# Kernel tuning notes

Hardware: AMD Instinct MI355X
Metric: run time of the kernel (lower is better)

The kernel has to match this reference:

```python
import jax, jax.numpy as jnp
import numpy as np

EPS = 1e-5
OFFSET_SCALE = 1.0
KPTS = 9   # 3x3 deformable kernel
GROUP = 1  # in_dim // out_dim


def _bn(x, g, b, m, v):
    # eval-mode BatchNorm2d on (B,C,H,W)
    s = g / jnp.sqrt(v + EPS)
    return x * s[None, :, None, None] + (b - m * s)[None, :, None, None]


def _dcnv4_core(value, offset, mask, offset_scale):
    # value: (B,H,W,G,Cg); offset: (B,H,W,G,K,2) as (dx,dy); mask: (B,H,W,G,K)
    B, H, W, G, Cg = value.shape
    K = mask.shape[-1]
    dt = value.dtype
    ky = jnp.repeat(jnp.arange(3) - 1, 3).astype(dt)
    kx = jnp.tile(jnp.arange(3) - 1, 3).astype(dt)
    grid = jnp.stack([kx, ky], -1)                                   # (K,2)
    base = jnp.stack(jnp.meshgrid(jnp.arange(W, dtype=dt),
                                  jnp.arange(H, dtype=dt),
                                  indexing='xy'), -1)                # (H,W,2) = (x,y)
    loc = base[None, :, :, None, None, :] + (grid + offset) * offset_scale  # (B,H,W,G,K,2)
    px, py = loc[..., 0], loc[..., 1]
    x0 = jnp.floor(px); y0 = jnp.floor(py)
    fx = px - x0; fy = py - y0
    vflat = value.transpose(0, 3, 1, 2, 4).reshape(B, G, H * W, Cg)
    out = jnp.zeros((B, G, H * W, Cg), dt)
    corners = ((0.0, 0.0, (1 - fx) * (1 - fy)), (1.0, 0.0, fx * (1 - fy)),
               (0.0, 1.0, (1 - fx) * fy), (1.0, 1.0, fx * fy))
    for dx, dy, wgt in corners:
        xi = x0 + dx; yi = y0 + dy
        valid = ((xi >= 0) & (xi < W) & (yi >= 0) & (yi < H)).astype(dt)
        idx = (jnp.clip(yi, 0, W and H - 1) * W + jnp.clip(xi, 0, W - 1)).astype(jnp.int32)
        idx = idx.transpose(0, 3, 1, 2, 4).reshape(B, G, H * W * K)
        v = jnp.take_along_axis(vflat, idx[..., None], axis=2).reshape(B, G, H * W, K, Cg)
        w = (wgt * valid * mask).transpose(0, 3, 1, 2, 4).reshape(B, G, H * W, K)
        out = out + jnp.einsum('bgsk,bgskc->bgsc', w, v)
    return out.reshape(B, G, H, W, Cg).transpose(0, 2, 3, 1, 4).reshape(B, H, W, G * Cg)


def setup_inputs() -> dict:
    key = jax.random.key(0)
    B, C, H, W = 8, 128, 64, 64
    C_OUT = 128
    OM = ((GROUP * KPTS * 3 + 7) // 8) * 8  # 32, offset_mask padded width
    ks = jax.random.split(key, 16)
    f = jnp.float32
    sc = 1.0 / np.sqrt(C).astype(np.float32)
    return {
        'x': jax.random.normal(ks[0], (B, C, H, W), f),
        'bn1_g': jax.random.uniform(ks[1], (C,), f, 0.5, 1.5),
        'bn1_b': jax.random.normal(ks[2], (C,), f) * 0.1,
        'bn1_m': jax.random.normal(ks[3], (C,), f) * 0.1,
        'bn1_v': jax.random.uniform(ks[4], (C,), f, 0.5, 1.5),
        'w_pw0': jax.random.normal(ks[5], (C, C), f) * sc,
        'w_vp': jax.random.normal(ks[6], (C, C), f) * sc,
        'b_vp': jnp.zeros((C,), f),
        'w_om': jax.random.normal(ks[7], (C, OM), f) * 0.01,
        'b_om': jnp.zeros((OM,), f),
        'w_op': jax.random.normal(ks[8], (C, C), f) * sc,
        'bn2_g': jax.random.uniform(ks[9], (C,), f, 0.5, 1.5),
        'bn2_b': jax.random.normal(ks[10], (C,), f) * 0.1,
        'bn2_m': jax.random.normal(ks[11], (C,), f) * 0.1,
        'bn2_v': jax.random.uniform(ks[12], (C,), f, 0.5, 1.5),
        'w_pw1': jax.random.normal(ks[13], (C_OUT, C), f) * sc,
    }


def reference(x, bn1_g, bn1_b, bn1_m, bn1_v, w_pw0, w_vp, b_vp, w_om, b_om, w_op,
              bn2_g, bn2_b, bn2_m, bn2_v, w_pw1):
    x = _bn(x, bn1_g, bn1_b, bn1_m, bn1_v)
    x = jnp.einsum('bchw,oc->bohw', x, w_pw0)
    B, C, H, W = x.shape
    x = x.reshape(B, H * W, C)  # raw reshape (faithful to torch .reshape, NOT a permute)
    G, K = GROUP, KPTS
    Cg = C // G
    value = (x @ w_vp + b_vp).reshape(B, H, W, G, Cg)
    om = (x @ w_om + b_om)[..., :G * K * 3].reshape(B, H, W, G, K, 3)
    out = _dcnv4_core(value, om[..., :2], om[..., 2], OFFSET_SCALE)
    out = out.reshape(B, H * W, C) @ w_op
    x = out.reshape(B, C, H, W)  # raw reshape back
    x = _bn(x, bn2_g, bn2_b, bn2_m, bn2_v)
    x = jnp.einsum('bchw,oc->bohw', x, w_pw1)
    return x
```

## Files before the change

### kernel.cpp

```cpp
#include <hip/hip_runtime.h>

#define HW 4096
#define PADF 33
#define PADU 136
typedef unsigned short ushort;
typedef __attribute__((ext_vector_type(8))) short short8;
typedef __attribute__((ext_vector_type(4))) float f32x4;

__device__ __forceinline__ ushort bf_rne(float f) {
  unsigned u = __float_as_uint(f);
  unsigned r = (u + 0x7fffu + ((u >> 16) & 1u)) >> 16;
  return (ushort)r;
}
__device__ __forceinline__ void split2(float f, ushort& hi, ushort& lo) {
  ushort h = bf_rne(f);
  float hf = __uint_as_float((unsigned)h << 16);
  hi = h;
  lo = bf_rne(f - hf);
}

__global__ __launch_bounds__(256) void prep(
    const float* __restrict__ g1, const float* __restrict__ be1,
    const float* __restrict__ m1, const float* __restrict__ v1,
    const float* __restrict__ w0,
    const float* __restrict__ g2, const float* __restrict__ be2,
    const float* __restrict__ m2, const float* __restrict__ v2,
    const float* __restrict__ w1,
    const float* __restrict__ wvp, const float* __restrict__ wom,
    const float* __restrict__ wop,
    ushort* __restrict__ W0h, ushort* __restrict__ W0l, float* __restrict__ b0,
    ushort* __restrict__ W1h, ushort* __restrict__ W1l, float* __restrict__ b1,
    ushort* __restrict__ vph, ushort* __restrict__ vpl,
    ushort* __restrict__ oph, ushort* __restrict__ opl,
    ushort* __restrict__ omh, ushort* __restrict__ oml)
{
  const int t = threadIdx.x;
  const int role = blockIdx.x;
  if (role < 16) {
    __shared__ float sc[128], sh[128], part[16][17];
    const int cv = role >> 3;
    const float* g  = cv ? g2 : g1;
    const float* be = cv ? be2 : be1;
    const float* mm = cv ? m2 : m1;
    const float* vv = cv ? v2 : v1;
    if (t < 128) {
      float s = g[t] / sqrtf(vv[t] + 1e-5f);
      sc[t] = s;
      sh[t] = be[t] - mm[t] * s;
    }
    __syncthreads();
    const float* ws = cv ? w1 : w0;
    ushort* dh = cv ? W1h : W0h;
    ushort* dl = cv ? W1l : W0l;
    float* bb  = cv ? b1 : b0;
    const int o = ((role & 7) << 4) + (t >> 4);
    const int kl = t & 15;
    float accb = 0.f;
    #pragma unroll
    for (int j = 0; j < 8; ++j) {
      const int k = (kl << 3) + j;
      const float wv = ws[o * 128 + k];
      ushort hi, lo;
      split2(wv * sc[k], hi, lo);
      dh[o * 128 + k] = hi;
      dl[o * 128 + k] = lo;
      accb = fmaf(wv, sh[k], accb);
    }
    part[t >> 4][kl] = accb;
    __syncthreads();
    if (kl == 0) {
      float s = 0.f;
      #pragma unroll
      for (int j = 0; j < 16; ++j) s += part[t >> 4][j];
      bb[o] = s;
    }
  } else if (role < 32) {
    const int rr = role & 7;
    const float* srcM = (role < 24) ? wvp : wop;
    ushort* dh = (role < 24) ? vph : oph;
    ushort* dl = (role < 24) ? vpl : opl;
    const int n = (rr << 4) + (t >> 4);
    const int kl = t & 15;
    #pragma unroll
    for (int j = 0; j < 8; ++j) {
      const int k = (kl << 3) + j;
      ushort hi, lo;
      split2(srcM[k * 128 + n], hi, lo);
      dh[n * 128 + k] = hi;
      dl[n * 128 + k] = lo;
    }
  } else {
    const int n = ((role - 32) << 4) + (t >> 4);
    const int kl = t & 15;
    #pragma unroll
    for (int j = 0; j < 8; ++j) {
      const int k = (kl << 3) + j;
      ushort hi, lo;
      split2(wom[k * 32 + n], hi, lo);
      omh[n * 128 + k] = hi;
      oml[n * 128 + k] = lo;
    }
  }
}

__global__ __launch_bounds__(256, 2) void fused_x_valom(
    const float* __restrict__ x,
    const ushort* __restrict__ W0h, const ushort* __restrict__ W0l,
    const float* __restrict__ b0,
    const ushort* __restrict__ vph, const ushort* __restrict__ vpl,
    const float* __restrict__ bvp, const float* __restrict__ bom,
    float* __restrict__ value, float* __restrict__ omb)
{
  __shared__ __align__(16) char smem[55296];
  __shared__ float b0_s[64], b2_s[160];
  ushort (*Wh_s)[32] = (ushort(*)[32])(smem);
  ushort (*Wl_s)[32] = (ushort(*)[32])(smem + 4096);
  float*  Xf         = (float*)(smem + 8192);
  ushort (*Yh)[PADU] = (ushort(*)[PADU])(smem);
  ushort (*Yl)[PADU] = (ushort(*)[PADU])(smem + 17408);
  ushort (*Vh_s)[32] = (ushort(*)[32])(smem + 34816);
  ushort (*Vl_s)[32] = (ushort(*)[32])(smem + 45056);

  const int t = threadIdx.x;
  const int cb = blockIdx.x;
  const int b  = blockIdx.y;
  const int oBase = blockIdx.z << 6;
  const int hwBase = cb << 7;
  const size_t xbase = (size_t)b * (size_t)(128 * HW);
  if (t < 64)  b0_s[t] = b0[oBase + t];
  if (t < 160) b2_s[t] = (t < 128) ? bvp[t] : bom[t - 128];
  const int lane = t & 63, w = t >> 6;
  const int col = lane & 15, quad = lane >> 4;
  const f32x4 z = {0.f, 0.f, 0.f, 0.f};

  f32x4 acc1[4][2];
  #pragma unroll
  for (int i = 0; i < 4; ++i) { acc1[i][0] = z; acc1[i][1] = z; }

  for (int kc = 0; kc < 4; ++kc) {
    const int kB = kc << 5;
    {
      const int o = t >> 2, q8 = (t & 3) << 3;
      *(uint4*)&Wh_s[o][q8] = *(const uint4*)&W0h[(oBase + o) * 128 + kB + q8];
      *(uint4*)&Wl_s[o][q8] = *(const uint4*)&W0l[(oBase + o) * 128 + kB + q8];
    }
    #pragma unroll
    for (int p = 0; p < 4; ++p) {
      const int idx = (p << 8) + t;
      const int c = idx >> 5, j4 = (idx & 31) << 2;
      const float4 f = *(const float4*)&x[xbase + (size_t)(kB + c) * HW + hwBase + j4];
      Xf[(j4 + 0) * PADF + c] = f.x;
      Xf[(j4 + 1) * PADF + c] = f.y;
      Xf[(j4 + 2) * PADF + c] = f.z;
      Xf[(j4 + 3) * PADF + c] = f.w;
    }
    __syncthreads();
    union { ushort u[8]; short8 v; } bh[2], bl[2];
    #pragma unroll
    for (int g = 0; g < 2; ++g) {
      const float* xr = &Xf[((w << 5) + (g << 4) + col) * PADF + (quad << 3)];
      #pragma unroll
      for (int j = 0; j < 8; ++j) split2(xr[j], bh[g].u[j], bl[g].u[j]);
    }
    #pragma unroll
    for (int f = 0; f < 4; ++f) {
      const int row = (f << 4) + col;
      const short8 aH = *(const short8*)&Wh_s[row][quad << 3];
      const short8 aL = *(const short8*)&Wl_s[row][quad << 3];
      #pragma unroll
      for (int g = 0; g < 2; ++g) {
        acc1[f][g] = __builtin_amdgcn_mfma_f32_16x16x32_bf16(aH, bh[g].v, acc1[f][g], 0, 0, 0);
        acc1[f][g] = __builtin_amdgcn_mfma_f32_16x16x32_bf16(aH, bl[g].v, acc1[f][g], 0, 0, 0);
        acc1[f][g] = __builtin_amdgcn_mfma_f32_16x16x32_bf16(aL, bh[g].v, acc1[f][g], 0, 0, 0);
      }
    }
    __syncthreads();
  }

  #pragma unroll
  for (int f = 0; f < 4; ++f)
    #pragma unroll
    for (int r = 0; r < 4; ++r) {
      const int m = (f << 4) + (quad << 2) + r;
      #pragma unroll
      for (int g = 0; g < 2; ++g) {
        const int j = (w << 5) + (g << 4) + col;
        ushort hi, lo;
        split2(acc1[f][g][r] + b0_s[m], hi, lo);
        Yh[m][j] = hi;
        Yl[m][j] = lo;
      }
    }

  const int wm2 = (w & 1) << 5;
  const int wn2 = (w >> 1) * 80;
  f32x4 acc2[2][5];
  #pragma unroll
  for (int i = 0; i < 2; ++i)
    #pragma unroll
    for (int j = 0; j < 5; ++j) acc2[i][j] = z;

  for (int j2 = 0; j2 < 4; ++j2) {
    for (int i = t; i < 640; i += 256) {
      const int n = i >> 2, q8 = (i & 3) << 3;
      *(uint4*)&Vh_s[n][q8] = *(const uint4*)&vph[n * 128 + (j2 << 5) + q8];
      *(uint4*)&Vl_s[n][q8] = *(const uint4*)&vpl[n * 128 + (j2 << 5) + q8];
    }
    __syncthreads();
    short8 aH[2], aL[2];
    #pragma unroll
    for (int f2 = 0; f2 < 2; ++f2) {
      const int row = wm2 + (f2 << 4) + col;
      aH[f2] = *(const short8*)&Yh[row][(j2 << 5) + (quad << 3)];
      aL[f2] = *(const short8*)&Yl[row][(j2 << 5) + (quad << 3)];
    }
    #pragma unroll
    for (int g2 = 0; g2 < 5; ++g2) {
      const int n = wn2 + (g2 << 4) + col;
      const short8 vh = *(const short8*)&Vh_s[n][quad << 3];
      const short8 vl = *(const short8*)&Vl_s[n][quad << 3];
      #pragma unroll
      for (int f2 = 0; f2 < 2; ++f2) {
        acc2[f2][g2] = __builtin_amdgcn_mfma_f32_16x16x32_bf16(aH[f2], vh, acc2[f2][g2], 0, 0, 0);
        acc2[f2][g2] = __builtin_amdgcn_mfma_f32_16x16x32_bf16(aH[f2], vl, acc2[f2][g2], 0, 0, 0);
        acc2[f2][g2] = __builtin_amdgcn_mfma_f32_16x16x32_bf16(aL[f2], vh, acc2[f2][g2], 0, 0, 0);
      }
    }
    __syncthreads();
  }
  #pragma unroll
  for (int f2 = 0; f2 < 2; ++f2)
    #pragma unroll
    for (int r = 0; r < 4; ++r) {
      const int m = wm2 + (f2 << 4) + (quad << 2) + r;
      const size_t gRow = (size_t)b * HW + (size_t)(oBase + m) * 32 + cb;
      #pragma unroll
      for (int g2 = 0; g2 < 5; ++g2) {
        const int n = wn2 + (g2 << 4) + col;
        const float v = acc2[f2][g2][r] + b2_s[n];
        if (n < 128) value[gRow * 128 + n] = v;
        else         omb[gRow * 32 + (n - 128)] = v;
      }
    }
}

__global__ __launch_bounds__(256) void dcn_sample(
    const float* __restrict__ value, const float* __restrict__ om,
    ushort* __restrict__ samph, ushort* __restrict__ sampl)
{
  __shared__ float oms[8][32];
  const int t = threadIdx.x;
  const int blk = blockIdx.x;
  const int b = blk & 7;
  const int sBase = (blk >> 3) << 3;
  const int s = sBase + (t >> 5);
  const int cg = (t & 31) << 2;
  oms[t >> 5][t & 31] = om[((size_t)b * HW + sBase + (t >> 5)) * 32 + (t & 31)];
  __syncthreads();
  const int h = s >> 6, wq = s & 63;
  const float* vb = value + (size_t)b * HW * 128;
  const float* omp = oms[t >> 5];
  const float fw = (float)wq, fh = (float)h;
  float4 acc = {0.f, 0.f, 0.f, 0.f};
  #pragma unroll
  for (int k = 0; k < 9; ++k) {
    const float kx = (float)(k % 3 - 1);
    const float ky = (float)(k / 3 - 1);
    const float dx = omp[k * 3 + 0];
    const float dy = omp[k * 3 + 1];
    const float m  = omp[k * 3 + 2];
    const float px = fw + kx + dx;
    const float py = fh + ky + dy;
    const float x0f = floorf(px), y0f = floorf(py);
    const float fx = px - x0f, fy = py - y0f;
    const int ix = (int)x0f, iy = (int)y0f;
    #pragma unroll
    for (int cy = 0; cy < 2; ++cy) {
      const int yi = iy + cy;
      const float wy = cy ? fy : 1.f - fy;
      const float vy = (yi >= 0 && yi < 64) ? 1.f : 0.f;
      const int yc = min(max(yi, 0), 63);
      #pragma unroll
      for (int cx = 0; cx < 2; ++cx) {
        const int xi = ix + cx;
        const float wx = cx ? fx : 1.f - fx;
        const float vx = (xi >= 0 && xi < 64) ? 1.f : 0.f;
        const int xc = min(max(xi, 0), 63);
        const float wgt = wx * wy * vx * vy * m;
        const float4 v = *(const float4*)&vb[(size_t)(yc * 64 + xc) * 128 + cg];
        acc.x = fmaf(wgt, v.x, acc.x);
        acc.y = fmaf(wgt, v.y, acc.y);
        acc.z = fmaf(wgt, v.z, acc.z);
        acc.w = fmaf(wgt, v.w, acc.w);
      }
    }
  }
  ushort h0, l0, h1, l1, h2, l2, h3, l3;
  split2(acc.x, h0, l0); split2(acc.y, h1, l1);
  split2(acc.z, h2, l2); split2(acc.w, h3, l3);
  const size_t idx = ((size_t)b * HW + s) * 128 + cg;
  uint2 uh, ul;
  uh.x = (unsigned)h0 | ((unsigned)h1 << 16);
  uh.y = (unsigned)h2 | ((unsigned)h3 << 16);
  ul.x = (unsigned)l0 | ((unsigned)l1 << 16);
  ul.y = (unsigned)l2 | ((unsigned)l3 << 16);
  *(uint2*)&samph[idx] = uh;
  *(uint2*)&sampl[idx] = ul;
}

__global__ __launch_bounds__(256, 2) void fused_op_out(
    const ushort* __restrict__ samph, const ushort* __restrict__ sampl,
    const ushort* __restrict__ oph, const ushort* __restrict__ opl,
    const ushort* __restrict__ W1h, const ushort* __restrict__ W1l,
    const float* __restrict__ b1, float* __restrict__ out)
{
  __shared__ __align__(16) char smem[51200];
  __shared__ float b1_s[128];
  ushort (*Ah_s)[32]  = (ushort(*)[32])(smem);
  ushort (*Al_s)[32]  = (ushort(*)[32])(smem + 8192);
  ushort (*Bh_s)[32]  = (ushort(*)[32])(smem + 16384);
  ushort (*Bl_s)[32]  = (ushort(*)[32])(smem + 20480);
  ushort (*Yh)[PADU]  = (ushort(*)[PADU])(smem);
  ushort (*Yl)[PADU]  = (ushort(*)[PADU])(smem + 17408);
  ushort (*W1h_s)[32] = (ushort(*)[32])(smem + 34816);
  ushort (*W1l_s)[32] = (ushort(*)[32])(smem + 43008);

  const int t = threadIdx.x;
  const int cb = blockIdx.x & 31;
  const int jBase = (blockIdx.x >> 5) << 6;
  const int b = blockIdx.y;
  if (t < 128) b1_s[t] = b1[t];
  const int lane = t & 63, w = t >> 6;
  const int col = lane & 15, quad = lane >> 4;
  const f32x4 z = {0.f, 0.f, 0.f, 0.f};

  const int wm1 = (w & 1) << 6, wn1 = (w >> 1) << 5;
  f32x4 acc1[4][2];
  #pragma unroll
  for (int i = 0; i < 4; ++i) { acc1[i][0] = z; acc1[i][1] = z; }

  for (int kc = 0; kc < 4; ++kc) {
    const int kB = kc << 5;
    for (int i = t; i < 512; i += 256) {
      const int m = i >> 2, q8 = (i & 3) << 3;
      const size_t row = (size_t)b * HW + (size_t)m * 32 + cb;
      *(uint4*)&Ah_s[m][q8] = *(const uint4*)&samph[row * 128 + kB + q8];
      *(uint4*)&Al_s[m][q8] = *(const uint4*)&sampl[row * 128 + kB + q8];
    }
    {
      const int n = t >> 2, q8 = (t & 3) << 3;
      *(uint4*)&Bh_s[n][q8] = *(const uint4*)&oph[(jBase + n) * 128 + kB + q8];
      *(uint4*)&Bl_s[n][q8] = *(const uint4*)&opl[(jBase + n) * 128 + kB + q8];
    }
    __syncthreads();
    short8 aH[4], aL[4];
    #pragma unroll
    for (int f = 0; f < 4; ++f) {
      const int row = wm1 + (f << 4) + col;
      aH[f] = *(const short8*)&Ah_s[row][quad << 3];
      aL[f] = *(const short8*)&Al_s[row][quad << 3];
    }
    #pragma unroll
    for (int g = 0; g < 2; ++g) {
      const int n = wn1 + (g << 4) + col;
      const short8 bh = *(const short8*)&Bh_s[n][quad << 3];
      const short8 bl = *(const short8*)&Bl_s[n][quad << 3];
      #pragma unroll
      for (int f = 0; f < 4; ++f) {
        acc1[f][g] = __builtin_amdgcn_mfma_f32_16x16x32_bf16(aH[f], bh, acc1[f][g], 0, 0, 0);
        acc1[f][g] = __builtin_amdgcn_mfma_f32_16x16x32_bf16(aH[f], bl, acc1[f][g], 0, 0, 0);
        acc1[f][g] = __builtin_amdgcn_mfma_f32_16x16x32_bf16(aL[f], bh, acc1[f][g], 0, 0, 0);
      }
    }
    __syncthreads();
  }

  #pragma unroll
  for (int f = 0; f < 4; ++f)
    #pragma unroll
    for (int g = 0; g < 2; ++g)
      #pragma unroll
      for (int r = 0; r < 4; ++r) {
        const int ch = wm1 + (f << 4) + (quad << 2) + r;
        const int j  = wn1 + (g << 4) + col;
        ushort hi, lo;
        split2(acc1[f][g][r], hi, lo);
        Yh[j][ch] = hi;
        Yl[j][ch] = lo;
      }

  const int wm2 = (w & 1) << 6, wn2 = (w >> 1) << 5;
  f32x4 acc2[4][2];
  #pragma unroll
  for (int i = 0; i < 4; ++i) { acc2[i][0] = z; acc2[i][1] = z; }

  for (int j2 = 0; j2 < 4; ++j2) {
    for (int i = t; i < 512; i += 256) {
      const int o = i >> 2, q8 = (i & 3) << 3;
      *(uint4*)&W1h_s[o][q8] = *(const uint4*)&W1h[o * 128 + (j2 << 5) + q8];
      *(uint4*)&W1l_s[o][q8] = *(const uint4*)&W1l[o * 128 + (j2 << 5) + q8];
    }
    __syncthreads();
    short8 aH[4], aL[4];
    #pragma unroll
    for (int f2 = 0; f2 < 4; ++f2) {
      const int row = wm2 + (f2 << 4) + col;
      aH[f2] = *(const short8*)&W1h_s[row][quad << 3];
      aL[f2] = *(const short8*)&W1l_s[row][quad << 3];
    }
    #pragma unroll
    for (int g2 = 0; g2 < 2; ++g2) {
      const int j = wn2 + (g2 << 4) + col;
      const short8 bh = *(const short8*)&Yh[j][(j2 << 5) + (quad << 3)];
      const short8 bl = *(const short8*)&Yl[j][(j2 << 5) + (quad << 3)];
      #pragma unroll
      for (int f2 = 0; f2 < 4; ++f2) {
        acc2[f2][g2] = __builtin_amdgcn_mfma_f32_16x16x32_bf16(aH[f2], bh, acc2[f2][g2], 0, 0, 0);
        acc2[f2][g2] = __builtin_amdgcn_mfma_f32_16x16x32_bf16(aH[f2], bl, acc2[f2][g2], 0, 0, 0);
        acc2[f2][g2] = __builtin_amdgcn_mfma_f32_16x16x32_bf16(aL[f2], bh, acc2[f2][g2], 0, 0, 0);
      }
    }
    __syncthreads();
  }
  const size_t obase = (size_t)b * (size_t)(128 * HW) + ((size_t)cb << 7) + jBase;
  #pragma unroll
  for (int f2 = 0; f2 < 4; ++f2)
    #pragma unroll
    for (int r = 0; r < 4; ++r) {
      const int o = wm2 + (f2 << 4) + (quad << 2) + r;
      #pragma unroll
      for (int g2 = 0; g2 < 2; ++g2) {
        const int j = wn2 + (g2 << 4) + col;
        out[obase + (size_t)o * HW + j] = acc2[f2][g2][r] + b1_s[o];
      }
    }
}

extern "C" void kernel_launch(void* const* d_in, const int* in_sizes, int n_in,
                              void* d_out, int out_size, void* d_ws, size_t ws_size,
                              hipStream_t stream)
{
  const float* x    = (const float*)d_in[0];
  const float* g1   = (const float*)d_in[1];
  const float* be1  = (const float*)d_in[2];
  const float* m1   = (const float*)d_in[3];
  const float* v1   = (const float*)d_in[4];
  const float* wpw0 = (const float*)d_in[5];
  const float* wvp  = (const float*)d_in[6];
  const float* bvp  = (const float*)d_in[7];
  const float* womW = (const float*)d_in[8];
  const float* bom  = (const float*)d_in[9];
  const float* wop  = (const float*)d_in[10];
  const float* g2   = (const float*)d_in[11];
  const float* be2  = (const float*)d_in[12];
  const float* m2   = (const float*)d_in[13];
  const float* v2   = (const float*)d_in[14];
  const float* wpw1 = (const float*)d_in[15];

  char* ws = (char*)d_ws;
  float*  value = (float*) (ws + 0);
  float*  omb   = (float*) (ws + 16777216);
  ushort* samph = (ushort*)(ws + 20971520);
  ushort* sampl = (ushort*)(ws + 29360128);
  size_t o = 37748736;
  ushort* W0h = (ushort*)(ws + o); o += 32768;
  ushort* W0l = (ushort*)(ws + o); o += 32768;
  ushort* W1h = (ushort*)(ws + o); o += 32768;
  ushort* W1l = (ushort*)(ws + o); o += 32768;
  ushort* vph = (ushort*)(ws + o); o += 40960;
  ushort* vpl = (ushort*)(ws + o); o += 40960;
  ushort* oph = (ushort*)(ws + o); o += 32768;
  ushort* opl = (ushort*)(ws + o); o += 32768;
  float*  b0  = (float*)(ws + o);  o += 512;
  float*  b1  = (float*)(ws + o);
  ushort* omh = vph + 128 * 128;
  ushort* oml = vpl + 128 * 128;

  prep<<<34, 256, 0, stream>>>(g1, be1, m1, v1, wpw0, g2, be2, m2, v2, wpw1,
                               wvp, womW, wop,
                               W0h, W0l, b0, W1h, W1l, b1,
                               vph, vpl, oph, opl, omh, oml);
  fused_x_valom<<<dim3(32, 8, 2), 256, 0, stream>>>(x, W0h, W0l, b0, vph, vpl,
                                                    bvp, bom, value, omb);
  dcn_sample<<<dim3(4096), 256, 0, stream>>>(value, omb, samph, sampl);
  fused_op_out<<<dim3(64, 8), 256, 0, stream>>>(samph, sampl, oph, opl,
                                                W1h, W1l, b1, (float*)d_out);
}
```

Measured before the change: 148.6 us.

## Precompute bilinear corner weights/offsets in shared memory and widen dcn_sample blocks

The sampling kernel now runs in two phases. First, 288 threads each compute one (pixel, kernel point, corner) weight and offset into shared memory. Then 512 threads, 64 per pixel with 2 channels each, gather and accumulate, skipping corners whose weight is zero. This removes the redundant coordinate math every channel thread used to repeat and adds more threads per block, at the cost of float2 instead of float4 loads, an extra barrier and a data-dependent branch.

```diff
diff --git a/kernel.cpp b/kernel.cpp
--- a/kernel.cpp
+++ b/kernel.cpp
@@ -244,68 +244,76 @@
     }
 }
 
-__global__ __launch_bounds__(256) void dcn_sample(
+__global__ __launch_bounds__(512) void dcn_sample(
     const float* __restrict__ value, const float* __restrict__ om,
     ushort* __restrict__ samph, ushort* __restrict__ sampl)
 {
   __shared__ float oms[8][32];
+  __shared__ float wg_s[72][4];
+  __shared__ int   of_s[72][4];
   const int t = threadIdx.x;
   const int blk = blockIdx.x;
   const int b = blk & 7;
   const int sBase = (blk >> 3) << 3;
-  const int s = sBase + (t >> 5);
-  const int cg = (t & 31) << 2;
-  oms[t >> 5][t & 31] = om[((size_t)b * HW + sBase + (t >> 5)) * 32 + (t & 31)];
+  const int h = sBase >> 6;
+  const float* vb = value + (size_t)b * HW * 128;
+
+  if (t < 256)
+    oms[t >> 5][t & 31] = om[((size_t)b * HW + sBase + (t >> 5)) * 32 + (t & 31)];
   __syncthreads();
-  const int h = s >> 6, wq = s & 63;
-  const float* vb = value + (size_t)b * HW * 128;
-  const float* omp = oms[t >> 5];
-  const float fw = (float)wq, fh = (float)h;
-  float4 acc = {0.f, 0.f, 0.f, 0.f};
-  #pragma unroll
-  for (int k = 0; k < 9; ++k) {
+
+  if (t < 288) {
+    const int sk = t >> 2, c = t & 3;
+    const int sl = sk / 9, k = sk - sl * 9;
+    const float* omp = oms[sl];
     const float kx = (float)(k % 3 - 1);
     const float ky = (float)(k / 3 - 1);
     const float dx = omp[k * 3 + 0];
     const float dy = omp[k * 3 + 1];
     const float m  = omp[k * 3 + 2];
+    const float fw = (float)((sBase & 63) + sl);
+    const float fh = (float)h;
     const float px = fw + kx + dx;
     const float py = fh + ky + dy;
     const float x0f = floorf(px), y0f = floorf(py);
     const float fx = px - x0f, fy = py - y0f;
     const int ix = (int)x0f, iy = (int)y0f;
-    #pragma unroll
-    for (int cy = 0; cy < 2; ++cy) {
-      const int yi = iy + cy;
-      const float wy = cy ? fy : 1.f - fy;
-      const float vy = (yi >= 0 && yi < 64) ? 1.f : 0.f;
-      const int yc = min(max(yi, 0), 63);
-      #pragma unroll
-      for (int cx = 0; cx < 2; ++cx) {
-        const int xi = ix + cx;
-        const float wx = cx ? fx : 1.f - fx;
-        const float vx = (xi >= 0 && xi < 64) ? 1.f : 0.f;
-        const int xc = min(max(xi, 0), 63);
-        const float wgt = wx * wy * vx * vy * m;
-        const float4 v = *(const float4*)&vb[(size_t)(yc * 64 + xc) * 128 + cg];
-        acc.x = fmaf(wgt, v.x, acc.x);
-        acc.y = fmaf(wgt, v.y, acc.y);
-        acc.z = fmaf(wgt, v.z, acc.z);
-        acc.w = fmaf(wgt, v.w, acc.w);
-      }
-    }
-  }
-  ushort h0, l0, h1, l1, h2, l2, h3, l3;
-  split2(acc.x, h0, l0); split2(acc.y, h1, l1);
-  split2(acc.z, h2, l2); split2(acc.w, h3, l3);
-  const size_t idx = ((size_t)b * HW + s) * 128 + cg;
-  uint2 uh, ul;
-  uh.x = (unsigned)h0 | ((unsigned)h1 << 16);
-  uh.y = (unsigned)h2 | ((unsigned)h3 << 16);
-  ul.x = (unsigned)l0 | ((unsigned)l1 << 16);
-  ul.y = (unsigned)l2 | ((unsigned)l3 << 16);
-  *(uint2*)&samph[idx] = uh;
-  *(uint2*)&sampl[idx] = ul;
+    const int cy = c >> 1, cx = c & 1;
+    const int yi = iy + cy, xi = ix + cx;
+    const float wy = cy ? fy : 1.f - fy;
+    const float wx = cx ? fx : 1.f - fx;
+    const float vy = (yi >= 0 && yi < 64) ? 1.f : 0.f;
+    const float vx = (xi >= 0 && xi < 64) ? 1.f : 0.f;
+    const int yc = min(max(yi, 0), 63);
+    const int xc = min(max(xi, 0), 63);
+    wg_s[sk][c] = wx * wy * vx * vy * m;
+    of_s[sk][c] = (yc * 64 + xc) * 128;
+  }
+  __syncthreads();
+
+  const int sl = t >> 6, lane = t & 63;
+  const int ch = lane << 1;
+  const float* vbc = vb + ch;
+  float a0 = 0.f, a1 = 0.f;
+  #pragma unroll
+  for (int k = 0; k < 9; ++k) {
+    const int sk = sl * 9 + k;
+    #pragma unroll
+    for (int c = 0; c < 4; ++c) {
+      const float wgt = wg_s[sk][c];
+      if (wgt != 0.f) {
+        const float2 v = *(const float2*)(vbc + of_s[sk][c]);
+        a0 = fmaf(wgt, v.x, a0);
+        a1 = fmaf(wgt, v.y, a1);
+      }
+    }
+  }
+  ushort h0, l0, h1, l1;
+  split2(a0, h0, l0);
+  split2(a1, h1, l1);
+  const size_t idx = ((size_t)b * HW + sBase + sl) * 128 + ch;
+  *(unsigned*)&samph[idx] = (unsigned)h0 | ((unsigned)h1 << 16);
+  *(unsigned*)&sampl[idx] = (unsigned)l0 | ((unsigned)l1 << 16);
 }
 
 __global__ __launch_bounds__(256, 2) void fused_op_out(
@@ -482,7 +490,7 @@
                                vph, vpl, oph, opl, omh, oml);
   fused_x_valom<<<dim3(32, 8, 2), 256, 0, stream>>>(x, W0h, W0l, b0, vph, vpl,
                                                     bvp, bom, value, omb);
-  dcn_sample<<<dim3(4096), 256, 0, stream>>>(value, omb, samph, sampl);
+  dcn_sample<<<dim3(4096), 512, 0, stream>>>(value, omb, samph, sampl);
   fused_op_out<<<dim3(64, 8), 256, 0, stream>>>(samph, sampl, oph, opl,
                                                 W1h, W1l, b1, (float*)d_out);
 }
```

New measurement: 171.2 us. 1.15x slower.
